# Performance work log

Hardware: AMD Instinct MI355X
Metric: run time of the kernel (lower is better)

## Reference

```python
import jax, jax.numpy as jnp
import numpy as np

N_FFT = 512
HOP = 160
N_ITER = 32
PAD = N_FFT // 2
TWO_PI = 2.0 * np.pi


def _stft(x, window):
    # x: [B, L] real -> spec [B, T, F] complex, center=True reflect pad (torch.stft)
    xp = jnp.pad(x, ((0, 0), (PAD, PAD)), mode='reflect')
    T = 1 + (xp.shape[-1] - N_FFT) // HOP
    idx = jnp.arange(T)[:, None] * HOP + jnp.arange(N_FFT)[None, :]  # [T, n_fft]
    frames = xp[:, idx] * window  # [B, T, n_fft]
    return jnp.fft.rfft(frames, axis=-1)  # [B, T, F]


def _istft(spec, window):
    # spec: [B, T, F] complex -> waveform [B, (T-1)*HOP] (torch.istft, center=True, length=None)
    frames = jnp.fft.irfft(spec, n=N_FFT, axis=-1) * window  # [B, T, n_fft]
    B, T, _ = frames.shape
    out_len = N_FFT + HOP * (T - 1)
    idx = (jnp.arange(T)[:, None] * HOP + jnp.arange(N_FFT)[None, :]).reshape(-1)
    y = jnp.zeros((B, out_len), frames.dtype).at[:, idx].add(frames.reshape(B, -1))
    wsq = jnp.zeros((out_len,), window.dtype).at[idx].add(jnp.tile(window * window, T))
    y = y / jnp.where(wsq > 1e-11, wsq, 1.0)  # NOLA normalization
    return y[:, PAD:out_len - PAD]


def setup_inputs() -> dict:
    key = jax.random.key(0)
    k1, k2 = jax.random.split(key)
    magnitude = jax.random.uniform(k1, (32, 1024, 257), dtype=jnp.float32)
    angles_init = jax.random.normal(k2, (32, 1024, 257), dtype=jnp.float32) * TWO_PI
    # hann window, periodic (torch.hann_window default)
    window = (0.5 * (1.0 - jnp.cos(TWO_PI * jnp.arange(N_FFT) / N_FFT))).astype(jnp.float32)
    return {"magnitude": magnitude, "angles_init": angles_init, "window": window}


def reference(magnitude, angles_init, window):
    # magnitude: [B, T, F]. Internally we keep [B, T, F] layout (torch transposes to
    # [B, F, T] before stft/istft; the math is identical, only the layout differs).
    mag = magnitude

    def step(angles, _):
        spec = mag * (jnp.cos(angles) + 1j * jnp.sin(angles))  # mag * exp(i*angles)
        wav = _istft(spec, window)
        rec = _stft(wav, window)
        new_angles = jnp.arctan2(rec.imag, rec.real)  # torch.angle
        return new_angles, None

    angles, _ = jax.lax.scan(step, angles_init, None, length=N_ITER)
    final_spec = mag * (jnp.cos(angles) + 1j * jnp.sin(angles))
    return _istft(final_spec, window)  # [B, (T-1)*HOP] = [32, 163680]
```

## Files before the change

kernel.cpp:

```cpp
#include <hip/hip_runtime.h>
#include <math.h>

#define BATCH 32
#define TFRAMES 1024
#define NBINS 257
#define NFFT 512
#define HOP 160
#define LOUT 163680
#define XPLEN 164192
#define NITER 32
#define FPW 4
#define WSTRIDE (FPW*HOP)
#define BSTRIDE (2*WSTRIDE)
#define HALO (NFFT-HOP)
#define WSPAN (WSTRIDE+HALO)
#define SPAN (BSTRIDE+HALO)
#define NBLK 128
#define SLOT SPAN
#define SB ((size_t)NBLK*SLOT)
#define SBUF ((size_t)BATCH*SB)

#define P(i) ((i) + ((i) >> 5))

__device__ __forceinline__ float cosr(float x){ return __builtin_amdgcn_cosf(x); }
__device__ __forceinline__ float sinr(float x){ return __builtin_amdgcn_sinf(x); }
__device__ __forceinline__ void wsync(){
    __builtin_amdgcn_fence(__ATOMIC_SEQ_CST, "wavefront");
    __builtin_amdgcn_wave_barrier();
}

struct Tw { float c1,s1,c2,s2,c3,s3; };
__device__ __forceinline__ Tw twset(float x){
    Tw t; float c=cosr(x), s=sinr(x);
    t.c1=c; t.s1=s;
    t.c2=c*c-s*s; t.s2=2.f*c*s;
    t.c3=t.c2*c-t.s2*s; t.s3=t.c2*s+t.s2*c;
    return t;
}

template<int SIGN, bool TWID>
__device__ __forceinline__ void bfly4(const float xr[4], const float xi[4],
                                      const Tw& t, float yr[4], float yi[4]){
    constexpr float SG = (SIGN>0)?1.f:-1.f;
    float apc_r=xr[0]+xr[2], apc_i=xi[0]+xi[2];
    float amc_r=xr[0]-xr[2], amc_i=xi[0]-xi[2];
    float bpd_r=xr[1]+xr[3], bpd_i=xi[1]+xi[3];
    float bmd_r=xr[1]-xr[3], bmd_i=xi[1]-xi[3];
    yr[0]=apc_r+bpd_r; yi[0]=apc_i+bpd_i;
    float u2r=apc_r-bpd_r, u2i=apc_i-bpd_i;
    float u1r=amc_r-SG*bmd_i, u1i=amc_i+SG*bmd_r;
    float u3r=amc_r+SG*bmd_i, u3i=amc_i-SG*bmd_r;
    if (TWID){
        float s1=SG*t.s1, s2=SG*t.s2, s3=SG*t.s3;
        yr[1]=t.c1*u1r-s1*u1i; yi[1]=t.c1*u1i+s1*u1r;
        yr[2]=t.c2*u2r-s2*u2i; yi[2]=t.c2*u2i+s2*u2r;
        yr[3]=t.c3*u3r-s3*u3i; yi[3]=t.c3*u3i+s3*u3r;
    } else {
        yr[1]=u1r; yi[1]=u1i; yr[2]=u2r; yi[2]=u2i; yr[3]=u3r; yi[3]=u3i;
    }
}

template<int SIGN>
__device__ __forceinline__ void fft256reg(float xr[4], float xi[4],
                                          float* br, float* bi,
                                          const Tw& tw0, const Tw& tw1, const Tw& tw2,
                                          int lane){
    float yr[4], yi[4], ar[4], ai[4];
    bfly4<SIGN,true>(xr, xi, tw0, yr, yi);
    { int o = 4*lane;
#pragma unroll
      for (int c=0;c<4;++c){ br[P(o+c)]=yr[c]; bi[P(o+c)]=yi[c]; } }
    wsync();
#pragma unroll
    for (int c=0;c<4;++c){ ar[c]=br[P(lane+64*c)]; ai[c]=bi[P(lane+64*c)]; }
    wsync();
    bfly4<SIGN,true>(ar, ai, tw1, yr, yi);
    { int o = (lane&3) + 16*(lane>>2);
#pragma unroll
      for (int c=0;c<4;++c){ br[P(o+4*c)]=yr[c]; bi[P(o+4*c)]=yi[c]; } }
    wsync();
#pragma unroll
    for (int c=0;c<4;++c){ ar[c]=br[P(lane+64*c)]; ai[c]=bi[P(lane+64*c)]; }
    wsync();
    bfly4<SIGN,true>(ar, ai, tw2, yr, yi);
    { int o = (lane&15) + 64*(lane>>4);
#pragma unroll
      for (int c=0;c<4;++c){ br[P(o+16*c)]=yr[c]; bi[P(o+16*c)]=yi[c]; } }
    wsync();
#pragma unroll
    for (int c=0;c<4;++c){ ar[c]=br[P(lane+64*c)]; ai[c]=bi[P(lane+64*c)]; }
    wsync();
    bfly4<SIGN,false>(ar, ai, tw0, xr, xi);
}

__global__ __launch_bounds__(256) void k_init(const float* __restrict__ win,
                                              float* __restrict__ wsqi){
    int i = blockIdx.x*256 + threadIdx.x;
    if (i < XPLEN){
        int n = i;
        int tmax = n / HOP; if (tmax > TFRAMES-1) tmax = TFRAMES-1;
        int tmin = (n - (NFFT-1) + (HOP-1)) / HOP; if (tmin < 0) tmin = 0;
        float acc = 0.f;
        for (int t = tmin; t <= tmax; ++t){ float w = win[n - t*HOP]; acc += w*w; }
        wsqi[i] = 1.0f / (acc > 1e-11f ? acc : 1.0f);
    }
}

__device__ __forceinline__ float xs(const float* __restrict__ Sb,
                                    const float* __restrict__ wsq, int p){
    int bxp = p / BSTRIDE, r = p - bxp*BSTRIDE;
    float a = 0.f;
    if (bxp < NBLK) a = Sb[(size_t)bxp*SLOT + r];
    if (r < HALO && bxp > 0) a += Sb[(size_t)(bxp-1)*SLOT + BSTRIDE + r];
    return a * wsq[p];
}
__device__ __forceinline__ float2 xs2(const float* __restrict__ Sb,
                                      const float* __restrict__ wsq, int p){
    int bxp = p / BSTRIDE, r = p - bxp*BSTRIDE;
    float2 acc = make_float2(0.f, 0.f);
    if (bxp < NBLK) acc = *(const float2*)(Sb + (size_t)bxp*SLOT + r);
    if (r < HALO && bxp > 0){
        float2 h = *(const float2*)(Sb + (size_t)(bxp-1)*SLOT + BSTRIDE + r);
        acc.x += h.x; acc.y += h.y;
    }
    float2 q = *(const float2*)(wsq + p);
    return make_float2(acc.x*q.x, acc.y*q.y);
}

__device__ __forceinline__ void inv_accum(float pr[4], float pi[4],
                                          float* br, float* bi,
                                          const Tw& tw0, const Tw& tw1, const Tw& tw2,
                                          const float wA[4], const float wB[4],
                                          int lane, int f, float2* sa2){
    fft256reg<+1>(pr, pi, br, bi, tw0, tw1, tw2, lane);
    constexpr float SC = 1.f/256.f;
    int base2 = f*(HOP/2);
#pragma unroll
    for (int c=0;c<4;++c){
        int u = base2 + lane + 64*c;
        float2 v = sa2[u];
        v.x += pr[c]*wA[c]*SC;
        v.y += pi[c]*wB[c]*SC;
        sa2[u] = v;
    }
    wsync();
}

__device__ __forceinline__ void slot_store(float* __restrict__ Sw, int b, int bx,
                                           const float* s0, const float* s1, int tid){
    float2* slot2 = (float2*)(Sw + ((size_t)b*NBLK + bx)*SLOT);
    const float2* s0_2 = (const float2*)s0;
    const float2* s1_2 = (const float2*)s1;
#pragma unroll
    for (int j=0;j<7;++j){
        int u = tid + 128*j;
        if (u < SPAN/2){
            float2 v = make_float2(0.f, 0.f);
            if (u < WSPAN/2) v = s0_2[u];
            if (u >= WSTRIDE/2){
                float2 w1 = s1_2[u - WSTRIDE/2];
                v.x += w1.x; v.y += w1.y;
            }
            slot2[u] = v;
        }
    }
}

__global__ __launch_bounds__(128,4) void k_gl(const float* __restrict__ Sr,
                                              float* __restrict__ Sw,
                                              const float* __restrict__ mag,
                                              const float* __restrict__ win,
                                              const float* __restrict__ wsq){
    __shared__ __align__(16) float sacc[2][WSPAN];
    __shared__ __align__(16) float FR[2][272], FI[2][272];
    int tid = threadIdx.x, w = tid>>6, lane = tid&63;
    int b = blockIdx.y, bx = blockIdx.x;

    float *br = FR[w], *bi = FI[w];
    float2* sa2 = (float2*)sacc[w];

    Tw tw0 = twset((float)lane * (1.f/256.f));
    Tw tw1 = twset((float)(lane>>2) * (1.f/64.f));
    Tw tw2 = twset((float)(lane>>4) * (1.f/16.f));
    float twc[4], tws[4], wA[4], wB[4];
#pragma unroll
    for (int c=0;c<4;++c){
        int k = lane + 64*c;
        float x = (float)k * (1.f/512.f);
        twc[c]=cosr(x); tws[c]=sinr(x);
        float2 wv = ((const float2*)win)[k];
        wA[c]=wv.x; wB[c]=wv.y;
    }
#pragma unroll
    for (int j=0;j<8;++j){ int u = lane + 64*j; if (u < WSPAN/2) sa2[u]=make_float2(0.f,0.f); }
    __syncthreads();

    const float* Sb = Sr + (size_t)b*SB;
    const float* magb = mag + ((size_t)b*TFRAMES)*NBINS;
    int t0 = (bx*2 + w)*FPW;

#pragma unroll 1
    for (int f=0; f<FPW; ++f){
        int t = t0 + f;
        float fr[4], fi[4];
        bool edge = (t < 2) | (t >= TFRAMES-2);
        if (!edge){
            int pb = t*HOP;
#pragma unroll
            for (int c=0;c<4;++c){
                int p = pb + 2*(lane + 64*c);
                float2 v = xs2(Sb, wsq, p);
                fr[c] = v.x*wA[c];
                fi[c] = v.y*wB[c];
            }
        } else {
#pragma unroll
            for (int c=0;c<4;++c){
                int m = lane + 64*c;
                int p0 = t*HOP + 2*m, p1 = p0+1;
                int n0 = (p0<256)?(512-p0):((p0>=LOUT+256)?(2*LOUT+510-p0):p0);
                int n1 = (p1<256)?(512-p1):((p1>=LOUT+256)?(2*LOUT+510-p1):p1);
                fr[c] = xs(Sb, wsq, n0)*wA[c];
                fi[c] = xs(Sb, wsq, n1)*wB[c];
            }
        }
        fft256reg<-1>(fr, fi, br, bi, tw0, tw1, tw2, lane);
        wsync();
#pragma unroll
        for (int c=0;c<4;++c){ int k=lane+64*c; br[P(k)]=fr[c]; bi[P(k)]=fi[c]; }
        wsync();
        float pr[4], pi[4];
        const float* magp = magb + (size_t)t*NBINS;
#pragma unroll
        for (int c=0;c<4;++c){
            int k = lane + 64*c;
            int mk = (256 - k) & 255;
            float yr = br[P(mk)], yi = bi[P(mk)];
            float zr = fr[c], zi = fi[c];
            float Xer = 0.5f*(zr+yr), Xei = 0.5f*(zi-yi);
            float Dr = zr-yr, Di = zi+yi;
            float Xor = 0.5f*Di, Xoi = -0.5f*Dr;
            float Or = twc[c]*Xor + tws[c]*Xoi;
            float Oi = twc[c]*Xoi - tws[c]*Xor;
            float X1r = Xer + Or, X1i = Xei + Oi;
            float X2r = Xer - Or, X2i = Oi - Xei;
            float q1 = X1r*X1r + X1i*X1i;
            bool ok1 = q1 > 1e-30f;
            float v1 = ok1 ? __builtin_amdgcn_rsqf(q1) : 0.f;
            float c1 = ok1 ? X1r*v1 : 1.f, s1 = X1i*v1;
            float q2 = X2r*X2r + X2i*X2i;
            bool ok2 = q2 > 1e-30f;
            float v2 = ok2 ? __builtin_amdgcn_rsqf(q2) : 0.f;
            float c2 = ok2 ? X2r*v2 : 1.f, s2 = X2i*v2;
            float m1 = magp[k], m2 = magp[256-k];
            float S1r = m1*c1, S1i = m1*s1;
            float S2r = m2*c2, S2i = m2*s2;
            float Aer = 0.5f*(S1r+S2r), Aei = 0.5f*(S1i-S2i);
            float Er = S1r - S2r, Ei = S1i + S2i;
            float Bor = 0.5f*(twc[c]*Er - tws[c]*Ei);
            float Boi = 0.5f*(twc[c]*Ei + tws[c]*Er);
            pr[c] = Aer - Boi;
            pi[c] = Aei + Bor;
        }
        wsync();
        inv_accum(pr, pi, br, bi, tw0, tw1, tw2, wA, wB, lane, f, sa2);
    }
    __syncthreads();
    slot_store(Sw, b, bx, sacc[0], sacc[1], tid);
}

__global__ __launch_bounds__(128,4) void k_inv0s(const float* __restrict__ mag,
                                                 const float* __restrict__ ang,
                                                 const float* __restrict__ win,
                                                 float* __restrict__ Sw){
    __shared__ __align__(16) float sacc[2][WSPAN];
    __shared__ __align__(16) float FR[2][272], FI[2][272];
    int tid = threadIdx.x, w = tid>>6, lane = tid&63;
    int b = blockIdx.y, bx = blockIdx.x;

    float *br = FR[w], *bi = FI[w];
    float2* sa2 = (float2*)sacc[w];

    Tw tw0 = twset((float)lane * (1.f/256.f));
    Tw tw1 = twset((float)(lane>>2) * (1.f/64.f));
    Tw tw2 = twset((float)(lane>>4) * (1.f/16.f));
    float twc[4], tws[4], wA[4], wB[4];
#pragma unroll
    for (int c=0;c<4;++c){
        int k = lane + 64*c;
        float x = (float)k * (1.f/512.f);
        twc[c]=cosr(x); tws[c]=sinr(x);
        float2 wv = ((const float2*)win)[k];
        wA[c]=wv.x; wB[c]=wv.y;
    }
#pragma unroll
    for (int j=0;j<8;++j){ int u = lane + 64*j; if (u < WSPAN/2) sa2[u]=make_float2(0.f,0.f); }
    __syncthreads();

    const float* magb = mag + ((size_t)b*TFRAMES)*NBINS;
    const float* angb = ang + ((size_t)b*TFRAMES)*NBINS;
    int t0 = (bx*2 + w)*FPW;

#pragma unroll 1
    for (int f=0; f<FPW; ++f){
        int t = t0 + f;
        const float* magp = magb + (size_t)t*NBINS;
        const float* angp = angb + (size_t)t*NBINS;
        float sr_[4], si_[4];
#pragma unroll
        for (int c=0;c<4;++c){
            int k = lane + 64*c;
            float m = magp[k], a = angp[k];
            float sn, cs;
            sincosf(a, &sn, &cs);
            sr_[c] = m*cs;
            si_[c] = (c==0 && lane==0) ? 0.f : m*sn;
        }
#pragma unroll
        for (int c=0;c<4;++c){ int k=lane+64*c; br[P(k)]=sr_[c]; bi[P(k)]=si_[c]; }
        if (lane==0){
            br[P(256)] = magp[256]*cosf(angp[256]);
            bi[P(256)] = 0.f;
        }
        wsync();
        float pr[4], pi[4];
#pragma unroll
        for (int c=0;c<4;++c){
            int k = lane + 64*c;
            float yr = br[P(256-k)], yi = bi[P(256-k)];
            float Aer = 0.5f*(sr_[c]+yr), Aei = 0.5f*(si_[c]-yi);
            float Er = sr_[c]-yr, Ei = si_[c]+yi;
            float Bor = 0.5f*(twc[c]*Er - tws[c]*Ei);
            float Boi = 0.5f*(twc[c]*Ei + tws[c]*Er);
            pr[c] = Aer - Boi;
            pi[c] = Aei + Bor;
        }
        wsync();
        inv_accum(pr, pi, br, bi, tw0, tw1, tw2, wA, wB, lane, f, sa2);
    }
    __syncthreads();
    slot_store(Sw, b, bx, sacc[0], sacc[1], tid);
}

__global__ __launch_bounds__(128) void k_out(const float* __restrict__ S,
                                             const float* __restrict__ wsq,
                                             float* __restrict__ out){
    int b = blockIdx.y;
    int idx = blockIdx.x*128 + threadIdx.x;
    if (idx >= LOUT/2) return;
    const float* Sb = S + (size_t)b*SB;
    float2 v = xs2(Sb, wsq, 256 + 2*idx);
    ((float2*)(out + (size_t)b*LOUT))[idx] = v;
}

extern "C" void kernel_launch(void* const* d_in, const int* in_sizes, int n_in,
                              void* d_out, int out_size, void* d_ws, size_t ws_size,
                              hipStream_t stream) {
    const float* mag  = (const float*)d_in[0];
    const float* ang0 = (const float*)d_in[1];
    const float* win  = (const float*)d_in[2];
    float* ws = (float*)d_ws;
    float* S[2] = { ws, ws + SBUF };
    float* wsqi = ws + 2*SBUF;
    float* outp = (float*)d_out;

    k_init<<<(XPLEN + 255)/256, 256, 0, stream>>>(win, wsqi);

    dim3 g(NBLK, BATCH);
    k_inv0s<<<g, 128, 0, stream>>>(mag, ang0, win, S[0]);
    for (int it = 0; it < NITER; ++it){
        k_gl<<<g, 128, 0, stream>>>(S[it%2], S[(it+1)%2], mag, win, wsqi);
    }
    k_out<<<dim3(640, BATCH), 128, 0, stream>>>(S[NITER%2], wsqi, outp);
}
```

Measured before the change: 1.492 ms.

## Replace LDS-based 256-point FFT with register FFT using DPP swizzles and bpermute

In the main Griffin-Lim kernel, the shared-memory staged radix-4 FFT is replaced by one radix-4 stage followed by a 64-point in-register FFT per column. The column FFT exchanges data across lanes with ds_swizzle and ds_bpermute, and the mirrored-bin lookup for the real-FFT split is done with bpermute in bit-reversed order. The inverse transform runs the same exchanges in reverse, and the magnitude loads are hoisted ahead of the FFT. This removes the per-wave LDS FFT buffers and their wave syncs, at the cost of more cross-lane instructions and more twiddle registers held per lane.

```diff
diff --git a/kernel.cpp b/kernel.cpp
--- a/kernel.cpp
+++ b/kernel.cpp
@@ -27,6 +27,10 @@
 __device__ __forceinline__ void wsync(){
     __builtin_amdgcn_fence(__ATOMIC_SEQ_CST, "wavefront");
     __builtin_amdgcn_wave_barrier();
+}
+#define SWZ(v, d) __int_as_float(__builtin_amdgcn_ds_swizzle(__float_as_int(v), (((d)<<10)|0x1F)))
+__device__ __forceinline__ float bperm(int addr, float v){
+    return __int_as_float(__builtin_amdgcn_ds_bpermute(addr, __float_as_int(v)));
 }
 
 struct Tw { float c1,s1,c2,s2,c3,s3; };
@@ -60,6 +64,63 @@
     }
 }
 
+struct LTw {
+    float c32,t32,c16,t16,c8,t8,c4,t4,c2,t2;
+    float g32,g16,g8,g4,g2,g1;
+};
+__device__ __forceinline__ LTw ltw_init(int l){
+    LTw L; float t;
+    t = (l&32)? (float)(l&31)*(1.f/64.f) : 0.f; L.c32=cosr(t); L.t32=-sinr(t);
+    t = (l&16)? (float)(l&15)*(1.f/32.f) : 0.f; L.c16=cosr(t); L.t16=-sinr(t);
+    t = (l&8) ? (float)(l&7) *(1.f/16.f) : 0.f; L.c8 =cosr(t); L.t8 =-sinr(t);
+    t = (l&4) ? (float)(l&3) *(1.f/8.f)  : 0.f; L.c4 =cosr(t); L.t4 =-sinr(t);
+    t = (l&2) ? (float)(l&1) *(1.f/4.f)  : 0.f; L.c2 =cosr(t); L.t2 =-sinr(t);
+    L.g32=(l&32)?-1.f:1.f; L.g16=(l&16)?-1.f:1.f; L.g8=(l&8)?-1.f:1.f;
+    L.g4 =(l&4) ?-1.f:1.f; L.g2 =(l&2) ?-1.f:1.f; L.g1=(l&1)?-1.f:1.f;
+    return L;
+}
+
+__device__ __forceinline__ void f64fwd(float& r, float& i, const LTw& L, int a32){
+    float vr, vi, ur, ui;
+    vr = bperm(a32, r); vi = bperm(a32, i);
+    ur = fmaf(L.g32, r, vr); ui = fmaf(L.g32, i, vi);
+    r = L.c32*ur - L.t32*ui; i = L.c32*ui + L.t32*ur;
+    vr = SWZ(r,16); vi = SWZ(i,16);
+    ur = fmaf(L.g16, r, vr); ui = fmaf(L.g16, i, vi);
+    r = L.c16*ur - L.t16*ui; i = L.c16*ui + L.t16*ur;
+    vr = SWZ(r,8); vi = SWZ(i,8);
+    ur = fmaf(L.g8, r, vr); ui = fmaf(L.g8, i, vi);
+    r = L.c8*ur - L.t8*ui; i = L.c8*ui + L.t8*ur;
+    vr = SWZ(r,4); vi = SWZ(i,4);
+    ur = fmaf(L.g4, r, vr); ui = fmaf(L.g4, i, vi);
+    r = L.c4*ur - L.t4*ui; i = L.c4*ui + L.t4*ur;
+    vr = SWZ(r,2); vi = SWZ(i,2);
+    ur = fmaf(L.g2, r, vr); ui = fmaf(L.g2, i, vi);
+    r = L.c2*ur - L.t2*ui; i = L.c2*ui + L.t2*ur;
+    vr = SWZ(r,1); vi = SWZ(i,1);
+    r = fmaf(L.g1, r, vr); i = fmaf(L.g1, i, vi);
+}
+__device__ __forceinline__ void f64inv(float& r, float& i, const LTw& L, int a32){
+    float vr, vi, ur, ui;
+    vr = SWZ(r,1); vi = SWZ(i,1);
+    r = fmaf(L.g1, r, vr); i = fmaf(L.g1, i, vi);
+    ur = L.c2*r + L.t2*i; ui = L.c2*i - L.t2*r;
+    vr = SWZ(ur,2); vi = SWZ(ui,2);
+    r = fmaf(L.g2, ur, vr); i = fmaf(L.g2, ui, vi);
+    ur = L.c4*r + L.t4*i; ui = L.c4*i - L.t4*r;
+    vr = SWZ(ur,4); vi = SWZ(ui,4);
+    r = fmaf(L.g4, ur, vr); i = fmaf(L.g4, ui, vi);
+    ur = L.c8*r + L.t8*i; ui = L.c8*i - L.t8*r;
+    vr = SWZ(ur,8); vi = SWZ(ui,8);
+    r = fmaf(L.g8, ur, vr); i = fmaf(L.g8, ui, vi);
+    ur = L.c16*r + L.t16*i; ui = L.c16*i - L.t16*r;
+    vr = SWZ(ur,16); vi = SWZ(ui,16);
+    r = fmaf(L.g16, ur, vr); i = fmaf(L.g16, ui, vi);
+    ur = L.c32*r + L.t32*i; ui = L.c32*i - L.t32*r;
+    vr = bperm(a32, ur); vi = bperm(a32, ui);
+    r = fmaf(L.g32, ur, vr); i = fmaf(L.g32, ui, vi);
+}
+
 template<int SIGN>
 __device__ __forceinline__ void fft256reg(float xr[4], float xi[4],
                                           float* br, float* bi,
@@ -172,28 +233,28 @@
                                               const float* __restrict__ win,
                                               const float* __restrict__ wsq){
     __shared__ __align__(16) float sacc[2][WSPAN];
-    __shared__ __align__(16) float FR[2][272], FI[2][272];
     int tid = threadIdx.x, w = tid>>6, lane = tid&63;
     int b = blockIdx.y, bx = blockIdx.x;
-
-    float *br = FR[w], *bi = FI[w];
     float2* sa2 = (float2*)sacc[w];
 
     Tw tw0 = twset((float)lane * (1.f/256.f));
-    Tw tw1 = twset((float)(lane>>2) * (1.f/64.f));
-    Tw tw2 = twset((float)(lane>>4) * (1.f/16.f));
-    float twc[4], tws[4], wA[4], wB[4];
-#pragma unroll
-    for (int c=0;c<4;++c){
-        int k = lane + 64*c;
-        float x = (float)k * (1.f/512.f);
-        twc[c]=cosr(x); tws[c]=sinr(x);
-        float2 wv = ((const float2*)win)[k];
-        wA[c]=wv.x; wB[c]=wv.y;
+    LTw L = ltw_init(lane);
+    int a32 = (lane^32) << 2;
+    int a63 = (lane^63) << 2;
+    int mrev = (int)(__builtin_bitreverse32((unsigned)lane) >> 26);
+    int mm = (64 - mrev) & 63;
+    int a0 = (int)((__builtin_bitreverse32((unsigned)mm) >> 26) << 2);
+    int k1[4]; float twc[4], tws[4], wA[4], wB[4];
+#pragma unroll
+    for (int j=0;j<4;++j){
+        k1[j] = 4*mrev + j;
+        float x = (float)k1[j] * (1.f/512.f);
+        twc[j]=cosr(x); tws[j]=sinr(x);
+        float2 wv = ((const float2*)win)[lane + 64*j];
+        wA[j]=wv.x; wB[j]=wv.y;
     }
 #pragma unroll
     for (int j=0;j<8;++j){ int u = lane + 64*j; if (u < WSPAN/2) sa2[u]=make_float2(0.f,0.f); }
-    __syncthreads();
 
     const float* Sb = Sr + (size_t)b*SB;
     const float* magb = mag + ((size_t)b*TFRAMES)*NBINS;
@@ -202,6 +263,11 @@
 #pragma unroll 1
     for (int f=0; f<FPW; ++f){
         int t = t0 + f;
+        const float* magp = magb + (size_t)t*NBINS;
+        float m1[4], m2[4];
+#pragma unroll
+        for (int j=0;j<4;++j){ m1[j] = magp[k1[j]]; m2[j] = magp[256 - k1[j]]; }
+
         float fr[4], fi[4];
         bool edge = (t < 2) | (t >= TFRAMES-2);
         if (!edge){
@@ -224,24 +290,24 @@
                 fi[c] = xs(Sb, wsq, n1)*wB[c];
             }
         }
-        fft256reg<-1>(fr, fi, br, bi, tw0, tw1, tw2, lane);
-        wsync();
-#pragma unroll
-        for (int c=0;c<4;++c){ int k=lane+64*c; br[P(k)]=fr[c]; bi[P(k)]=fi[c]; }
-        wsync();
+        float ur[4], ui[4];
+        bfly4<-1,true>(fr, fi, tw0, ur, ui);
+#pragma unroll
+        for (int j=0;j<4;++j) f64fwd(ur[j], ui[j], L, a32);
+        float yr[4], yi[4];
+        yr[0]=bperm(a0,  ur[0]); yi[0]=bperm(a0,  ui[0]);
+        yr[1]=bperm(a63, ur[3]); yi[1]=bperm(a63, ui[3]);
+        yr[2]=bperm(a63, ur[2]); yi[2]=bperm(a63, ui[2]);
+        yr[3]=bperm(a63, ur[1]); yi[3]=bperm(a63, ui[1]);
         float pr[4], pi[4];
-        const float* magp = magb + (size_t)t*NBINS;
-#pragma unroll
-        for (int c=0;c<4;++c){
-            int k = lane + 64*c;
-            int mk = (256 - k) & 255;
-            float yr = br[P(mk)], yi = bi[P(mk)];
-            float zr = fr[c], zi = fi[c];
-            float Xer = 0.5f*(zr+yr), Xei = 0.5f*(zi-yi);
-            float Dr = zr-yr, Di = zi+yi;
+#pragma unroll
+        for (int j=0;j<4;++j){
+            float zr = ur[j], zi = ui[j];
+            float Xer = 0.5f*(zr+yr[j]), Xei = 0.5f*(zi-yi[j]);
+            float Dr = zr-yr[j], Di = zi+yi[j];
             float Xor = 0.5f*Di, Xoi = -0.5f*Dr;
-            float Or = twc[c]*Xor + tws[c]*Xoi;
-            float Oi = twc[c]*Xoi - tws[c]*Xor;
+            float Or = twc[j]*Xor + tws[j]*Xoi;
+            float Oi = twc[j]*Xoi - tws[j]*Xor;
             float X1r = Xer + Or, X1i = Xei + Oi;
             float X2r = Xer - Or, X2i = Oi - Xei;
             float q1 = X1r*X1r + X1i*X1i;
@@ -252,18 +318,34 @@
             bool ok2 = q2 > 1e-30f;
             float v2 = ok2 ? __builtin_amdgcn_rsqf(q2) : 0.f;
             float c2 = ok2 ? X2r*v2 : 1.f, s2 = X2i*v2;
-            float m1 = magp[k], m2 = magp[256-k];
-            float S1r = m1*c1, S1i = m1*s1;
-            float S2r = m2*c2, S2i = m2*s2;
+            float S1r = m1[j]*c1, S1i = m1[j]*s1;
+            float S2r = m2[j]*c2, S2i = m2[j]*s2;
             float Aer = 0.5f*(S1r+S2r), Aei = 0.5f*(S1i-S2i);
             float Er = S1r - S2r, Ei = S1i + S2i;
-            float Bor = 0.5f*(twc[c]*Er - tws[c]*Ei);
-            float Boi = 0.5f*(twc[c]*Ei + tws[c]*Er);
-            pr[c] = Aer - Boi;
-            pi[c] = Aei + Bor;
-        }
-        wsync();
-        inv_accum(pr, pi, br, bi, tw0, tw1, tw2, wA, wB, lane, f, sa2);
+            float Bor = 0.5f*(twc[j]*Er - tws[j]*Ei);
+            float Boi = 0.5f*(twc[j]*Ei + tws[j]*Er);
+            pr[j] = Aer - Boi;
+            pi[j] = Aei + Bor;
+        }
+#pragma unroll
+        for (int j=0;j<4;++j) f64inv(pr[j], pi[j], L, a32);
+        float tr[4], ti[4];
+        tr[0]=pr[0]; ti[0]=pi[0];
+        tr[1]=tw0.c1*pr[1]-tw0.s1*pi[1]; ti[1]=tw0.c1*pi[1]+tw0.s1*pr[1];
+        tr[2]=tw0.c2*pr[2]-tw0.s2*pi[2]; ti[2]=tw0.c2*pi[2]+tw0.s2*pr[2];
+        tr[3]=tw0.c3*pr[3]-tw0.s3*pi[3]; ti[3]=tw0.c3*pi[3]+tw0.s3*pr[3];
+        float zr2[4], zi2[4];
+        bfly4<+1,false>(tr, ti, tw0, zr2, zi2);
+        constexpr float SC = 1.f/256.f;
+        int base2 = f*(HOP/2);
+#pragma unroll
+        for (int q=0;q<4;++q){
+            int u = base2 + lane + 64*q;
+            float2 v = sa2[u];
+            v.x += zr2[q]*wA[q]*SC;
+            v.y += zi2[q]*wB[q]*SC;
+            sa2[u] = v;
+        }
     }
     __syncthreads();
     slot_store(Sw, b, bx, sacc[0], sacc[1], tid);
```

New measurement: 1.772 ms. 1.19x slower.

## Process two frames per wave concurrently to interleave FFT stages

Applied to the files above, without the earlier changes.

Restructures the Griffin-Lim kernel loop so each wave handles two STFT frames per iteration, running their forward and inverse 256-point FFTs together through a dual-frame routine with separate LDS buffers. This halves the number of wave barriers per frame and gives more independent instructions to hide LDS and global load latency. In exchange it raises register pressure and LDS usage, which may hurt occupancy under launch_bounds(128,4). The overlap-add accumulation is inlined and split into two serialized updates.

```diff
diff --git a/kernel.cpp b/kernel.cpp
--- a/kernel.cpp
+++ b/kernel.cpp
@@ -93,6 +93,50 @@
     bfly4<SIGN,false>(ar, ai, tw0, xr, xi);
 }
 
+template<int SIGN>
+__device__ __forceinline__ void fft256_x2(float x0r[4], float x0i[4], float* b0r, float* b0i,
+                                          float x1r[4], float x1i[4], float* b1r, float* b1i,
+                                          const Tw& tw0, const Tw& tw1, const Tw& tw2,
+                                          int lane){
+    float y0r[4], y0i[4], y1r[4], y1i[4];
+    float a0r[4], a0i[4], a1r[4], a1i[4];
+    bfly4<SIGN,true>(x0r, x0i, tw0, y0r, y0i);
+    bfly4<SIGN,true>(x1r, x1i, tw0, y1r, y1i);
+    { int o = 4*lane;
+#pragma unroll
+      for (int c=0;c<4;++c){ b0r[P(o+c)]=y0r[c]; b0i[P(o+c)]=y0i[c];
+                             b1r[P(o+c)]=y1r[c]; b1i[P(o+c)]=y1i[c]; } }
+    wsync();
+#pragma unroll
+    for (int c=0;c<4;++c){ int u=P(lane+64*c);
+        a0r[c]=b0r[u]; a0i[c]=b0i[u]; a1r[c]=b1r[u]; a1i[c]=b1i[u]; }
+    wsync();
+    bfly4<SIGN,true>(a0r, a0i, tw1, y0r, y0i);
+    bfly4<SIGN,true>(a1r, a1i, tw1, y1r, y1i);
+    { int o = (lane&3) + 16*(lane>>2);
+#pragma unroll
+      for (int c=0;c<4;++c){ int u=P(o+4*c);
+          b0r[u]=y0r[c]; b0i[u]=y0i[c]; b1r[u]=y1r[c]; b1i[u]=y1i[c]; } }
+    wsync();
+#pragma unroll
+    for (int c=0;c<4;++c){ int u=P(lane+64*c);
+        a0r[c]=b0r[u]; a0i[c]=b0i[u]; a1r[c]=b1r[u]; a1i[c]=b1i[u]; }
+    wsync();
+    bfly4<SIGN,true>(a0r, a0i, tw2, y0r, y0i);
+    bfly4<SIGN,true>(a1r, a1i, tw2, y1r, y1i);
+    { int o = (lane&15) + 64*(lane>>4);
+#pragma unroll
+      for (int c=0;c<4;++c){ int u=P(o+16*c);
+          b0r[u]=y0r[c]; b0i[u]=y0i[c]; b1r[u]=y1r[c]; b1i[u]=y1i[c]; } }
+    wsync();
+#pragma unroll
+    for (int c=0;c<4;++c){ int u=P(lane+64*c);
+        a0r[c]=b0r[u]; a0i[c]=b0i[u]; a1r[c]=b1r[u]; a1i[c]=b1i[u]; }
+    wsync();
+    bfly4<SIGN,false>(a0r, a0i, tw0, x0r, x0i);
+    bfly4<SIGN,false>(a1r, a1i, tw0, x1r, x1i);
+}
+
 __global__ __launch_bounds__(256) void k_init(const float* __restrict__ win,
                                               float* __restrict__ wsqi){
     int i = blockIdx.x*256 + threadIdx.x;
@@ -166,17 +210,83 @@
     }
 }
 
+__device__ __forceinline__ void load_frame(const float* __restrict__ Sb,
+                                           const float* __restrict__ wsq,
+                                           int t, int lane,
+                                           const float wA[4], const float wB[4],
+                                           float fr[4], float fi[4]){
+    bool edge = (t < 2) | (t >= TFRAMES-2);
+    if (!edge){
+        int pb = t*HOP;
+#pragma unroll
+        for (int c=0;c<4;++c){
+            int p = pb + 2*(lane + 64*c);
+            float2 v = xs2(Sb, wsq, p);
+            fr[c] = v.x*wA[c];
+            fi[c] = v.y*wB[c];
+        }
+    } else {
+#pragma unroll
+        for (int c=0;c<4;++c){
+            int m = lane + 64*c;
+            int p0 = t*HOP + 2*m, p1 = p0+1;
+            int n0 = (p0<256)?(512-p0):((p0>=LOUT+256)?(2*LOUT+510-p0):p0);
+            int n1 = (p1<256)?(512-p1):((p1>=LOUT+256)?(2*LOUT+510-p1):p1);
+            fr[c] = xs(Sb, wsq, n0)*wA[c];
+            fi[c] = xs(Sb, wsq, n1)*wB[c];
+        }
+    }
+}
+
+__device__ __forceinline__ void spectral(const float fr[4], const float fi[4],
+                                         const float yr[4], const float yi[4],
+                                         const float* __restrict__ magp,
+                                         const float twc[4], const float tws[4],
+                                         int lane, float pr[4], float pi[4]){
+#pragma unroll
+    for (int c=0;c<4;++c){
+        int k = lane + 64*c;
+        float zr = fr[c], zi = fi[c];
+        float Xer = 0.5f*(zr+yr[c]), Xei = 0.5f*(zi-yi[c]);
+        float Dr = zr-yr[c], Di = zi+yi[c];
+        float Xor = 0.5f*Di, Xoi = -0.5f*Dr;
+        float Or = twc[c]*Xor + tws[c]*Xoi;
+        float Oi = twc[c]*Xoi - tws[c]*Xor;
+        float X1r = Xer + Or, X1i = Xei + Oi;
+        float X2r = Xer - Or, X2i = Oi - Xei;
+        float q1 = X1r*X1r + X1i*X1i;
+        bool ok1 = q1 > 1e-30f;
+        float v1 = ok1 ? __builtin_amdgcn_rsqf(q1) : 0.f;
+        float c1 = ok1 ? X1r*v1 : 1.f, s1 = X1i*v1;
+        float q2 = X2r*X2r + X2i*X2i;
+        bool ok2 = q2 > 1e-30f;
+        float v2 = ok2 ? __builtin_amdgcn_rsqf(q2) : 0.f;
+        float c2 = ok2 ? X2r*v2 : 1.f, s2 = X2i*v2;
+        float m1 = magp[k], m2 = magp[256-k];
+        float S1r = m1*c1, S1i = m1*s1;
+        float S2r = m2*c2, S2i = m2*s2;
+        float Aer = 0.5f*(S1r+S2r), Aei = 0.5f*(S1i-S2i);
+        float Er = S1r - S2r, Ei = S1i + S2i;
+        float Bor = 0.5f*(twc[c]*Er - tws[c]*Ei);
+        float Boi = 0.5f*(twc[c]*Ei + tws[c]*Er);
+        pr[c] = Aer - Boi;
+        pi[c] = Aei + Bor;
+    }
+}
+
 __global__ __launch_bounds__(128,4) void k_gl(const float* __restrict__ Sr,
                                               float* __restrict__ Sw,
                                               const float* __restrict__ mag,
                                               const float* __restrict__ win,
                                               const float* __restrict__ wsq){
     __shared__ __align__(16) float sacc[2][WSPAN];
-    __shared__ __align__(16) float FR[2][272], FI[2][272];
+    __shared__ __align__(16) float FRA[2][272], FIA[2][272];
+    __shared__ __align__(16) float FRB[2][272], FIB[2][272];
     int tid = threadIdx.x, w = tid>>6, lane = tid&63;
     int b = blockIdx.y, bx = blockIdx.x;
 
-    float *br = FR[w], *bi = FI[w];
+    float *bAr = FRA[w], *bAi = FIA[w];
+    float *bBr = FRB[w], *bBi = FIB[w];
     float2* sa2 = (float2*)sacc[w];
 
     Tw tw0 = twset((float)lane * (1.f/256.f));
@@ -200,70 +310,53 @@
     int t0 = (bx*2 + w)*FPW;
 
 #pragma unroll 1
-    for (int f=0; f<FPW; ++f){
-        int t = t0 + f;
-        float fr[4], fi[4];
-        bool edge = (t < 2) | (t >= TFRAMES-2);
-        if (!edge){
-            int pb = t*HOP;
-#pragma unroll
-            for (int c=0;c<4;++c){
-                int p = pb + 2*(lane + 64*c);
-                float2 v = xs2(Sb, wsq, p);
-                fr[c] = v.x*wA[c];
-                fi[c] = v.y*wB[c];
-            }
-        } else {
-#pragma unroll
-            for (int c=0;c<4;++c){
-                int m = lane + 64*c;
-                int p0 = t*HOP + 2*m, p1 = p0+1;
-                int n0 = (p0<256)?(512-p0):((p0>=LOUT+256)?(2*LOUT+510-p0):p0);
-                int n1 = (p1<256)?(512-p1):((p1>=LOUT+256)?(2*LOUT+510-p1):p1);
-                fr[c] = xs(Sb, wsq, n0)*wA[c];
-                fi[c] = xs(Sb, wsq, n1)*wB[c];
-            }
-        }
-        fft256reg<-1>(fr, fi, br, bi, tw0, tw1, tw2, lane);
-        wsync();
-#pragma unroll
-        for (int c=0;c<4;++c){ int k=lane+64*c; br[P(k)]=fr[c]; bi[P(k)]=fi[c]; }
-        wsync();
-        float pr[4], pi[4];
-        const float* magp = magb + (size_t)t*NBINS;
-#pragma unroll
-        for (int c=0;c<4;++c){
-            int k = lane + 64*c;
-            int mk = (256 - k) & 255;
-            float yr = br[P(mk)], yi = bi[P(mk)];
-            float zr = fr[c], zi = fi[c];
-            float Xer = 0.5f*(zr+yr), Xei = 0.5f*(zi-yi);
-            float Dr = zr-yr, Di = zi+yi;
-            float Xor = 0.5f*Di, Xoi = -0.5f*Dr;
-            float Or = twc[c]*Xor + tws[c]*Xoi;
-            float Oi = twc[c]*Xoi - tws[c]*Xor;
-            float X1r = Xer + Or, X1i = Xei + Oi;
-            float X2r = Xer - Or, X2i = Oi - Xei;
-            float q1 = X1r*X1r + X1i*X1i;
-            bool ok1 = q1 > 1e-30f;
-            float v1 = ok1 ? __builtin_amdgcn_rsqf(q1) : 0.f;
-            float c1 = ok1 ? X1r*v1 : 1.f, s1 = X1i*v1;
-            float q2 = X2r*X2r + X2i*X2i;
-            bool ok2 = q2 > 1e-30f;
-            float v2 = ok2 ? __builtin_amdgcn_rsqf(q2) : 0.f;
-            float c2 = ok2 ? X2r*v2 : 1.f, s2 = X2i*v2;
-            float m1 = magp[k], m2 = magp[256-k];
-            float S1r = m1*c1, S1i = m1*s1;
-            float S2r = m2*c2, S2i = m2*s2;
-            float Aer = 0.5f*(S1r+S2r), Aei = 0.5f*(S1i-S2i);
-            float Er = S1r - S2r, Ei = S1i + S2i;
-            float Bor = 0.5f*(twc[c]*Er - tws[c]*Ei);
-            float Boi = 0.5f*(twc[c]*Ei + tws[c]*Er);
-            pr[c] = Aer - Boi;
-            pi[c] = Aei + Bor;
-        }
-        wsync();
-        inv_accum(pr, pi, br, bi, tw0, tw1, tw2, wA, wB, lane, f, sa2);
+    for (int fp=0; fp<2; ++fp){
+        int tA = t0 + 2*fp, tB = tA + 1;
+        float fAr[4], fAi[4], fBr[4], fBi[4];
+        load_frame(Sb, wsq, tA, lane, wA, wB, fAr, fAi);
+        load_frame(Sb, wsq, tB, lane, wA, wB, fBr, fBi);
+
+        fft256_x2<-1>(fAr, fAi, bAr, bAi, fBr, fBi, bBr, bBi, tw0, tw1, tw2, lane);
+
+#pragma unroll
+        for (int c=0;c<4;++c){ int u=P(lane+64*c);
+            bAr[u]=fAr[c]; bAi[u]=fAi[c]; bBr[u]=fBr[c]; bBi[u]=fBi[c]; }
+        wsync();
+        float yAr[4], yAi[4], yBr[4], yBi[4];
+#pragma unroll
+        for (int c=0;c<4;++c){
+            int mk = (256 - (lane + 64*c)) & 255;
+            int u = P(mk);
+            yAr[c]=bAr[u]; yAi[c]=bAi[u]; yBr[c]=bBr[u]; yBi[c]=bBi[u];
+        }
+        wsync();
+
+        float pAr[4], pAi[4], pBr[4], pBi[4];
+        spectral(fAr, fAi, yAr, yAi, magb + (size_t)tA*NBINS, twc, tws, lane, pAr, pAi);
+        spectral(fBr, fBi, yBr, yBi, magb + (size_t)tB*NBINS, twc, tws, lane, pBr, pBi);
+
+        fft256_x2<+1>(pAr, pAi, bAr, bAi, pBr, pBi, bBr, bBi, tw0, tw1, tw2, lane);
+
+        constexpr float SC = 1.f/256.f;
+        int baseA = (2*fp)*(HOP/2), baseB = (2*fp+1)*(HOP/2);
+#pragma unroll
+        for (int c=0;c<4;++c){
+            int u = baseA + lane + 64*c;
+            float2 v = sa2[u];
+            v.x += pAr[c]*wA[c]*SC;
+            v.y += pAi[c]*wB[c]*SC;
+            sa2[u] = v;
+        }
+        wsync();
+#pragma unroll
+        for (int c=0;c<4;++c){
+            int u = baseB + lane + 64*c;
+            float2 v = sa2[u];
+            v.x += pBr[c]*wA[c]*SC;
+            v.y += pBi[c]*wB[c]*SC;
+            sa2[u] = v;
+        }
+        wsync();
     }
     __syncthreads();
     slot_store(Sw, b, bx, sacc[0], sacc[1], tid);
```

Measured after the change: 3.529 ms. 2.36x slower.
